# Kernel tuning notes

Measured on AMD Instinct MI355X. Metric: run time of the kernel, lower is better.

## Reference

```python
import jax, jax.numpy as jnp
import numpy as np

BS = 64          # BSR block size
B, D_IN, H, D_OUT = 4096, 1024, 4096, 1024
DENSITY = 0.5    # fraction of nonzero 64x64 blocks in fc2


def setup_inputs() -> dict:
    key = jax.random.key(0)
    ks = jax.random.split(key, 4)
    x = jax.random.normal(ks[0], (B, D_IN), jnp.float32)
    w1 = jax.random.normal(ks[1], (H, D_IN), jnp.float32) * (1.0 / np.sqrt(D_IN))
    b1 = jnp.zeros((H,), jnp.float32)
    w3 = jax.random.normal(ks[2], (D_OUT, H), jnp.float32) * (1.0 / np.sqrt(H))
    b3 = jnp.zeros((D_OUT,), jnp.float32)
    # Build BSR structure for fc2 weight [H, H]: block grid is (H//BS, H//BS)
    nbr, nbc = H // BS, H // BS
    rng = np.random.default_rng(0)
    mask = rng.random((nbr, nbc)) < DENSITY
    mask[:, 0] = True  # ensure each block row has at least one block
    crow = np.concatenate([[0], np.cumsum(mask.sum(axis=1))]).astype(np.int32)
    col = np.concatenate([np.nonzero(mask[r])[0] for r in range(nbr)]).astype(np.int32)
    nnzb = int(col.shape[0])
    values = jax.random.normal(ks[3], (nnzb, BS, BS), jnp.float32) * (1.0 / np.sqrt(H))
    return {
        "x": x, "w1": w1, "b1": b1,
        "values": values, "w3": w3, "b3": b3,
        "crow_indices": jnp.asarray(crow),
        "col_indices": jnp.asarray(col),
    }


def bsr_linear(x, crow, col, values, n_block_rows):
    """y = x @ W.T where W [out, in] is BSR with blocks values[nnzb, bs, bs]."""
    bsz = x.shape[0]
    bs = values.shape[1]
    nnzb = col.shape[0]
    # block row index of each nonzero block, from CSR row pointers
    block_row = jnp.searchsorted(crow, jnp.arange(nnzb, dtype=crow.dtype), side='right') - 1
    xb = x.reshape(bsz, -1, bs)            # [B, n_block_cols, bs]
    gath = xb[:, col]                      # [B, nnzb, bs] irregular gather
    # per-block contribution: block is W[row_blk, col_blk] of shape [bs_out, bs_in]
    contrib = jnp.einsum('bni,noi->nbo', gath, values)  # [nnzb, B, bs]
    yb = jax.ops.segment_sum(contrib, block_row, num_segments=n_block_rows)  # [nbr, B, bs]
    return yb.transpose(1, 0, 2).reshape(bsz, n_block_rows * bs)


def reference(x, w1, b1, values, w3, b3, crow_indices, col_indices):
    # Flatten is a no-op for 2D input
    h = jax.nn.relu(x @ w1.T + b1)                                   # fc1 + ReLU
    h = jax.nn.relu(bsr_linear(h, crow_indices, col_indices, values, H // BS))  # BSR fc2 + ReLU
    return h @ w3.T + b3                                             # fc3
```

## Files before the change

kernel.cpp:

```cpp
#include <hip/hip_runtime.h>
#include <hip/hip_bf16.h>
#include <stdint.h>


typedef __attribute__((ext_vector_type(4))) float f32x4;
typedef __attribute__((ext_vector_type(8))) __bf16 bf16x8;

#define DEV static __device__ __forceinline__

DEV ushort f2bf(float f) {
  union { float f; uint32_t u; } v; v.f = f;
  uint32_t r = v.u + 0x7fffu + ((v.u >> 16) & 1u);
  return (ushort)(r >> 16);
}

DEV void gld_lds16(const void* g, void* l) {
  __builtin_amdgcn_global_load_lds(
      (const __attribute__((address_space(1))) void*)g,
      (__attribute__((address_space(3))) void*)l, 16, 0, 0);
}

__global__ void cvt4_kernel(const float* __restrict__ s0, ushort* __restrict__ d0, int n0,
                            const float* __restrict__ s1, ushort* __restrict__ d1, int n1,
                            const float* __restrict__ s2, ushort* __restrict__ d2, int n2,
                            const float* __restrict__ s3, ushort* __restrict__ d3, int n3) {
  const int total = (n0 + n1 + n2 + n3) >> 2;
  for (int idx = blockIdx.x * blockDim.x + threadIdx.x; idx < total;
       idx += gridDim.x * blockDim.x) {
    int i = idx * 4;
    const float* s; ushort* d;
    if (i < n0)               { s = s0; d = d0; }
    else if ((i -= n0) < n1)  { s = s1; d = d1; }
    else if ((i -= n1) < n2)  { s = s2; d = d2; }
    else                      { i -= n2; s = s3; d = d3; }
    float4 v = *(const float4*)(s + i);
    ushort4 o;
    o.x = f2bf(v.x); o.y = f2bf(v.y); o.z = f2bf(v.z); o.w = f2bf(v.w);
    *(ushort4*)(d + i) = o;
  }
}

__global__ void combine_kernel(const float* __restrict__ p0, const float* __restrict__ p1,
                               const float* __restrict__ bias, float* __restrict__ out,
                               int total, int ncols) {
  int i = (blockIdx.x * blockDim.x + threadIdx.x) * 4;
  if (i >= total) return;
  float4 a = *(const float4*)(p0 + i);
  float4 b = *(const float4*)(p1 + i);
  const float4 bv = *(const float4*)(bias + (i & (ncols - 1)));
  a.x += b.x + bv.x; a.y += b.y + bv.y; a.z += b.z + bv.z; a.w += b.w + bv.w;
  *(float4*)(out + i) = a;
}

template <bool RELU, bool OUT_BF16>
__global__ __launch_bounds__(256)
void gemm_nt(const ushort* __restrict__ A, const ushort* __restrict__ W,
             const float* __restrict__ bias, void* __restrict__ Cv,
             int K, int lda, int ldw, int ldc) {
  __shared__ ushort As[128 * 64];
  __shared__ ushort Ws[128 * 64];
  const int tid = threadIdx.x;
  const int wid = tid >> 6, lane = tid & 63;
  const int wm = wid >> 1, wn = wid & 1;
  const int i0 = blockIdx.y * 128, j0 = blockIdx.x * 128;
  f32x4 acc[4][4] = {};

  const int lrow = lane >> 3;
  const int lcol = (lane & 7) * 16;

  for (int k0 = 0; k0 < K; k0 += 64) {
#pragma unroll
    for (int i = 0; i < 4; ++i) {
      int ch = wid * 4 + i;
      int row = ch * 8 + lrow;
      const char* ga = (const char*)A + ((size_t)(i0 + row) * lda + k0) * 2 + lcol;
      gld_lds16(ga, (char*)As + ch * 1024);
      const char* gw = (const char*)W + ((size_t)(j0 + row) * ldw + k0) * 2 + lcol;
      gld_lds16(gw, (char*)Ws + ch * 1024);
    }
    __syncthreads();
#pragma unroll
    for (int kk = 0; kk < 64; kk += 32) {
      const int cl = lane & 15;
      const int kg = kk + (lane >> 4) * 8;
      bf16x8 a[4], b[4];
#pragma unroll
      for (int m = 0; m < 4; ++m)
        a[m] = *(const bf16x8*)&As[(wm * 64 + m * 16 + cl) * 64 + kg];
#pragma unroll
      for (int n = 0; n < 4; ++n)
        b[n] = *(const bf16x8*)&Ws[(wn * 64 + n * 16 + cl) * 64 + kg];
#pragma unroll
      for (int m = 0; m < 4; ++m)
#pragma unroll
        for (int n = 0; n < 4; ++n)
          acc[m][n] = __builtin_amdgcn_mfma_f32_16x16x32_bf16(a[m], b[n], acc[m][n], 0, 0, 0);
    }
    __syncthreads();
  }

  const int cl = lane & 15, r4 = (lane >> 4) * 4;
#pragma unroll
  for (int n = 0; n < 4; ++n) {
    int col = j0 + wn * 64 + n * 16 + cl;
    float bv = bias ? bias[col] : 0.0f;
#pragma unroll
    for (int m = 0; m < 4; ++m) {
      int rowb = i0 + wm * 64 + m * 16 + r4;
#pragma unroll
      for (int r = 0; r < 4; ++r) {
        float v = acc[m][n][r] + bv;
        if (RELU) v = fmaxf(v, 0.0f);
        if (OUT_BF16)
          ((ushort*)Cv)[(size_t)(rowb + r) * ldc + col] = f2bf(v);
        else
          ((float*)Cv)[(size_t)(rowb + r) * ldc + col] = v;
      }
    }
  }
}

__global__ __launch_bounds__(256)
void gemm_nt_sk(const ushort* __restrict__ A, const ushort* __restrict__ W,
                float* __restrict__ P0, float* __restrict__ P1,
                int Khalf, int lda, int ldw, int ldc, int ntx) {
  const int kidx = blockIdx.x / ntx;
  const int bx = blockIdx.x % ntx;
  const ushort* Ao = A + (size_t)kidx * Khalf;
  const ushort* Wo = W + (size_t)kidx * Khalf;
  float* P = kidx ? P1 : P0;

  __shared__ ushort As[128 * 64];
  __shared__ ushort Ws[128 * 64];
  const int tid = threadIdx.x;
  const int wid = tid >> 6, lane = tid & 63;
  const int wm = wid >> 1, wn = wid & 1;
  const int i0 = blockIdx.y * 128, j0 = bx * 128;
  f32x4 acc[4][4] = {};

  const int lrow = lane >> 3;
  const int lcol = (lane & 7) * 16;

  for (int k0 = 0; k0 < Khalf; k0 += 64) {
#pragma unroll
    for (int i = 0; i < 4; ++i) {
      int ch = wid * 4 + i;
      int row = ch * 8 + lrow;
      const char* ga = (const char*)Ao + ((size_t)(i0 + row) * lda + k0) * 2 + lcol;
      gld_lds16(ga, (char*)As + ch * 1024);
      const char* gw = (const char*)Wo + ((size_t)(j0 + row) * ldw + k0) * 2 + lcol;
      gld_lds16(gw, (char*)Ws + ch * 1024);
    }
    __syncthreads();
#pragma unroll
    for (int kk = 0; kk < 64; kk += 32) {
      const int cl = lane & 15;
      const int kg = kk + (lane >> 4) * 8;
      bf16x8 a[4], b[4];
#pragma unroll
      for (int m = 0; m < 4; ++m)
        a[m] = *(const bf16x8*)&As[(wm * 64 + m * 16 + cl) * 64 + kg];
#pragma unroll
      for (int n = 0; n < 4; ++n)
        b[n] = *(const bf16x8*)&Ws[(wn * 64 + n * 16 + cl) * 64 + kg];
#pragma unroll
      for (int m = 0; m < 4; ++m)
#pragma unroll
        for (int n = 0; n < 4; ++n)
          acc[m][n] = __builtin_amdgcn_mfma_f32_16x16x32_bf16(a[m], b[n], acc[m][n], 0, 0, 0);
    }
    __syncthreads();
  }

  const int cl = lane & 15, r4 = (lane >> 4) * 4;
#pragma unroll
  for (int n = 0; n < 4; ++n) {
    int col = j0 + wn * 64 + n * 16 + cl;
#pragma unroll
    for (int m = 0; m < 4; ++m) {
      int rowb = i0 + wm * 64 + m * 16 + r4;
#pragma unroll
      for (int r = 0; r < 4; ++r)
        P[(size_t)(rowb + r) * ldc + col] = acc[m][n][r];
    }
  }
}

__global__ __launch_bounds__(256)
void bsr_gemm(const ushort* __restrict__ A, const ushort* __restrict__ V,
              const int* __restrict__ crow, const int* __restrict__ colind,
              ushort* __restrict__ C, int Hdim) {
  __shared__ ushort As[2][128 * 64];
  __shared__ ushort Vs[2][64 * 64];
  const int tid = threadIdx.x;
  const int wid = tid >> 6, lane = tid & 63;

  const int bid = blockIdx.x;
  const int xcd = bid & 7;
  const int j = bid >> 3;
  const int tile = xcd + 8 * (j & 3);
  const int br = j >> 2;
  const int i0 = tile * 128;

  f32x4 acc[2][4] = {};
  const int n0 = crow[br], n1 = crow[br + 1];

  const int lr = lane >> 3;
  const int gsw = ((lane & 7) ^ lr) * 16;

  auto stage = [&](int buf, int n) {
    const int c = colind[n];
    const char* Abase = (const char*)A + ((size_t)i0 * Hdim + (size_t)c * 64) * 2;
    const char* Vbase = (const char*)V + (size_t)n * 8192;
#pragma unroll
    for (int i = 0; i < 6; ++i) {
      int ch = wid * 6 + i;
      if (ch < 16) {
        int row = ch * 8 + lr;
        gld_lds16(Abase + (size_t)row * Hdim * 2 + gsw, (char*)As[buf] + ch * 1024);
      } else {
        int vch = ch - 16;
        gld_lds16(Vbase + (vch * 8 + lr) * 128 + gsw, (char*)Vs[buf] + vch * 1024);
      }
    }
  };

  auto compute = [&](int buf) {
#pragma unroll
    for (int kk = 0; kk < 64; kk += 32) {
      const int cl = lane & 15;
      const int kg = kk + (lane >> 4) * 8;
      const int kx = kg ^ ((cl & 7) << 3);
      bf16x8 a[2], b[4];
#pragma unroll
      for (int m = 0; m < 2; ++m)
        a[m] = *(const bf16x8*)&As[buf][(wid * 32 + m * 16 + cl) * 64 + kx];
#pragma unroll
      for (int nn = 0; nn < 4; ++nn)
        b[nn] = *(const bf16x8*)&Vs[buf][(nn * 16 + cl) * 64 + kx];
      __builtin_amdgcn_s_setprio(1);
#pragma unroll
      for (int m = 0; m < 2; ++m)
#pragma unroll
        for (int nn = 0; nn < 4; ++nn)
          acc[m][nn] = __builtin_amdgcn_mfma_f32_16x16x32_bf16(a[m], b[nn], acc[m][nn], 0, 0, 0);
      __builtin_amdgcn_s_setprio(0);
    }
  };

  int cur = 0;
  stage(0, n0);
  __syncthreads();
  for (int n = n0; n < n1; ++n) {
    if (n + 1 < n1) stage(cur ^ 1, n + 1);
    compute(cur);
    __syncthreads();
    cur ^= 1;
  }

  const int cl = lane & 15, r4 = (lane >> 4) * 4;
#pragma unroll
  for (int nn = 0; nn < 4; ++nn) {
    int col = br * 64 + nn * 16 + cl;
#pragma unroll
    for (int m = 0; m < 2; ++m) {
      int rowb = i0 + wid * 32 + m * 16 + r4;
#pragma unroll
      for (int r = 0; r < 4; ++r) {
        float v = fmaxf(acc[m][nn][r], 0.0f);
        C[(size_t)(rowb + r) * Hdim + col] = f2bf(v);
      }
    }
  }
}

extern "C" void kernel_launch(void* const* d_in, const int* in_sizes, int n_in,
                              void* d_out, int out_size, void* d_ws, size_t ws_size,
                              hipStream_t stream) {
  const float* x    = (const float*)d_in[0];
  const float* w1   = (const float*)d_in[1];
  const float* b1   = (const float*)d_in[2];
  const float* vals = (const float*)d_in[3];
  const float* w3   = (const float*)d_in[4];
  const float* b3   = (const float*)d_in[5];
  const int* crow   = (const int*)d_in[6];
  const int* colind = (const int*)d_in[7];

  const int Bb = 4096, Din = 1024, H = 4096, Dout = 1024;
  const int nnzb = in_sizes[7];

  char* ws = (char*)d_ws;
  size_t off = 0;
  ushort* xb  = (ushort*)(ws + off); off += (size_t)Bb * Din * 2;
  ushort* w1b = (ushort*)(ws + off); off += (size_t)H * Din * 2;
  ushort* w3b = (ushort*)(ws + off); off += (size_t)Dout * H * 2;
  ushort* vb  = (ushort*)(ws + off); off += (size_t)nnzb * 64 * 64 * 2;
  ushort* h1b = (ushort*)(ws + off); off += (size_t)Bb * H * 2;
  ushort* h2b = (ushort*)(ws + off); off += (size_t)Bb * H * 2;
  float* p0 = (float*)(ws + off); off += (size_t)Bb * Dout * 4;
  float* p1 = (float*)(ws + off); off += (size_t)Bb * Dout * 4;
  const bool can_splitk = (off <= ws_size);

  hipLaunchKernelGGL(cvt4_kernel, dim3(2048), dim3(256), 0, stream,
                     x,    xb,  Bb * Din,
                     w1,   w1b, H * Din,
                     w3,   w3b, Dout * H,
                     vals, vb,  nnzb * 4096);

  hipLaunchKernelGGL((gemm_nt<true, true>), dim3(H / 128, Bb / 128), dim3(256), 0, stream,
                     xb, w1b, b1, (void*)h1b, Din, Din, Din, H);
  hipLaunchKernelGGL(bsr_gemm, dim3((Bb / 128) * (H / 64)), dim3(256), 0, stream,
                     h1b, vb, crow, colind, h2b, H);
  if (can_splitk) {
    hipLaunchKernelGGL(gemm_nt_sk, dim3(2 * (Dout / 128), Bb / 128), dim3(256), 0, stream,
                       h2b, w3b, p0, p1, H / 2, H, H, Dout, Dout / 128);
    int total = Bb * Dout;
    hipLaunchKernelGGL(combine_kernel, dim3((total / 4 + 255) / 256), dim3(256), 0, stream,
                       p0, p1, b3, (float*)d_out, total, Dout);
  } else {
    hipLaunchKernelGGL((gemm_nt<false, false>), dim3(Dout / 128, Bb / 128), dim3(256), 0, stream,
                       h2b, w3b, b3, d_out, H, H, H, Dout);
  }
}
```

Baseline: 234.9 us.

## Triple-buffer BSR GEMM loads with fine-grained vmcnt waits and LDS column cache

The BSR fc2 kernel moves from double to triple buffering in LDS, prefetching two blocks ahead. It waits with explicit s_waitcnt vmcnt counts and a raw s_barrier instead of a full __syncthreads drain. Column indices are cached in LDS and per-chunk global offsets are precomputed to trim address arithmetic. The aim is to hide more global-load latency, at the cost of extra LDS (about 72KB), which may lower occupancy. Correctness also relies on exactly six loads per thread per stage.

```diff
diff --git a/kernel.cpp b/kernel.cpp
--- a/kernel.cpp
+++ b/kernel.cpp
@@ -190,8 +190,9 @@
 void bsr_gemm(const ushort* __restrict__ A, const ushort* __restrict__ V,
               const int* __restrict__ crow, const int* __restrict__ colind,
               ushort* __restrict__ C, int Hdim) {
-  __shared__ ushort As[2][128 * 64];
-  __shared__ ushort Vs[2][64 * 64];
+  __shared__ ushort As[3][128 * 64];
+  __shared__ ushort Vs[3][64 * 64];
+  __shared__ int colLds[64];
   const int tid = threadIdx.x;
   const int wid = tid >> 6, lane = tid & 63;
 
@@ -203,29 +204,38 @@
   const int i0 = tile * 128;
 
   f32x4 acc[2][4] = {};
-  const int n0 = crow[br], n1 = crow[br + 1];
+  const int n0 = crow[br];
+  const int nt = crow[br + 1] - n0;
+
+  if (tid < nt) colLds[tid] = colind[n0 + tid];
 
   const int lr = lane >> 3;
   const int gsw = ((lane & 7) ^ lr) * 16;
 
-  auto stage = [&](int buf, int n) {
-    const int c = colind[n];
-    const char* Abase = (const char*)A + ((size_t)i0 * Hdim + (size_t)c * 64) * 2;
-    const char* Vbase = (const char*)V + (size_t)n * 8192;
+  size_t gbase[6];
+  bool isA[6];
+#pragma unroll
+  for (int i = 0; i < 6; ++i) {
+    int ch = wid * 6 + i;
+    if (ch < 16) { isA[i] = true;  gbase[i] = (size_t)(i0 + ch * 8 + lr) * Hdim * 2 + gsw; }
+    else         { isA[i] = false; gbase[i] = (size_t)((ch - 16) * 8 + lr) * 128 + gsw; }
+  }
+
+  __syncthreads();
+
+  auto stage = [&](int slot, int n) {
+    const int c = colLds[n];
+    const size_t aoff = (size_t)c * 128;
+    const size_t voff = (size_t)(n0 + n) * 8192;
 #pragma unroll
     for (int i = 0; i < 6; ++i) {
       int ch = wid * 6 + i;
-      if (ch < 16) {
-        int row = ch * 8 + lr;
-        gld_lds16(Abase + (size_t)row * Hdim * 2 + gsw, (char*)As[buf] + ch * 1024);
-      } else {
-        int vch = ch - 16;
-        gld_lds16(Vbase + (vch * 8 + lr) * 128 + gsw, (char*)Vs[buf] + vch * 1024);
-      }
+      if (isA[i]) gld_lds16((const char*)A + gbase[i] + aoff, (char*)As[slot] + ch * 1024);
+      else        gld_lds16((const char*)V + gbase[i] + voff, (char*)Vs[slot] + (ch - 16) * 1024);
     }
   };
 
-  auto compute = [&](int buf) {
+  auto compute = [&](int slot) {
 #pragma unroll
     for (int kk = 0; kk < 64; kk += 32) {
       const int cl = lane & 15;
@@ -234,10 +244,10 @@
       bf16x8 a[2], b[4];
 #pragma unroll
       for (int m = 0; m < 2; ++m)
-        a[m] = *(const bf16x8*)&As[buf][(wid * 32 + m * 16 + cl) * 64 + kx];
+        a[m] = *(const bf16x8*)&As[slot][(wid * 32 + m * 16 + cl) * 64 + kx];
 #pragma unroll
       for (int nn = 0; nn < 4; ++nn)
-        b[nn] = *(const bf16x8*)&Vs[buf][(nn * 16 + cl) * 64 + kx];
+        b[nn] = *(const bf16x8*)&Vs[slot][(nn * 16 + cl) * 64 + kx];
       __builtin_amdgcn_s_setprio(1);
 #pragma unroll
       for (int m = 0; m < 2; ++m)
@@ -248,14 +258,23 @@
     }
   };
 
-  int cur = 0;
-  stage(0, n0);
-  __syncthreads();
-  for (int n = n0; n < n1; ++n) {
-    if (n + 1 < n1) stage(cur ^ 1, n + 1);
-    compute(cur);
-    __syncthreads();
-    cur ^= 1;
+  stage(0, 0);
+  if (nt > 1) {
+    stage(1, 1);
+    asm volatile("s_waitcnt vmcnt(6)" ::: "memory");
+  } else {
+    asm volatile("s_waitcnt vmcnt(0)" ::: "memory");
+  }
+  __builtin_amdgcn_s_barrier();
+
+  for (int n = 0; n < nt; ++n) {
+    if (n + 2 < nt) stage((n + 2) % 3, n + 2);
+    compute(n % 3);
+    if (n + 1 < nt) {
+      if (n + 2 < nt) asm volatile("s_waitcnt vmcnt(6)" ::: "memory");
+      else            asm volatile("s_waitcnt vmcnt(0)" ::: "memory");
+      __builtin_amdgcn_s_barrier();
+    }
   }
 
   const int cl = lane & 15, r4 = (lane >> 4) * 4;
```

Result: slower. 254.6 us (+8.4%).
